# Performance work log

Measured on AMD Instinct MI355X. Metric: run time of the kernel, lower is better.

## Reference

```python
import jax, jax.numpy as jnp
import numpy as np

B, T = 32, 1500
EPROJS, DUNITS = 1024, 1024
AHEADS, DK, DV = 8, 128, 128
SCALING = 1.0 / np.sqrt(DK)


def setup_inputs() -> dict:
    key = jax.random.key(0)
    ks = jax.random.split(key, 8)
    enc_hs_pad = jax.random.normal(ks[0], (B, T, EPROJS), dtype=jnp.float32)
    # lengths in [T//2, T] so every row has at least one valid frame
    enc_hs_len = jax.random.randint(ks[1], (B,), T // 2, T + 1, dtype=jnp.int64)
    dec_z = jax.random.normal(ks[2], (B, DUNITS), dtype=jnp.float32)
    # per-head projection weights (torch.nn.Linear default init scale ~ 1/sqrt(fan_in))
    Wq = jax.random.normal(ks[3], (AHEADS, DUNITS, DK), dtype=jnp.float32) / np.sqrt(DUNITS)
    bq = jax.random.normal(ks[4], (AHEADS, DK), dtype=jnp.float32) / np.sqrt(DUNITS)
    Wk = jax.random.normal(ks[5], (AHEADS, EPROJS, DK), dtype=jnp.float32) / np.sqrt(EPROJS)
    Wv = jax.random.normal(ks[6], (AHEADS, EPROJS, DV), dtype=jnp.float32) / np.sqrt(EPROJS)
    Wo = jax.random.normal(ks[7], (AHEADS * DV, EPROJS), dtype=jnp.float32) / np.sqrt(AHEADS * DV)
    return {"enc_hs_pad": enc_hs_pad, "enc_hs_len": enc_hs_len, "dec_z": dec_z,
            "Wq": Wq, "bq": bq, "Wk": Wk, "Wv": Wv, "Wo": Wo}


def reference(enc_hs_pad, enc_hs_len, dec_z, Wq, bq, Wk, Wv, Wo):
    # pre_compute_k / pre_compute_v, batched over heads
    k = jnp.tanh(jnp.einsum('btd,hdk->bhtk', enc_hs_pad, Wk))   # (B,H,T,DK)
    v = jnp.einsum('btd,hdv->bhtv', enc_hs_pad, Wv)             # (B,H,T,DV)
    q = jnp.tanh(jnp.einsum('bd,hdk->bhk', dec_z, Wq) + bq[None])  # (B,H,DK)
    e = jnp.einsum('bhtk,bhk->bht', k, q)                        # (B,H,T)
    # pad mask: positions >= length are masked with -inf (before scaling, as in source)
    pad = jnp.arange(T)[None, :] >= enc_hs_len[:, None]          # (B,T)
    e = jnp.where(pad[:, None, :], -jnp.inf, e)
    w = jax.nn.softmax(SCALING * e, axis=-1)                     # (B,H,T)
    c = jnp.einsum('bhtv,bht->bhv', v, w)                        # (B,H,DV)
    out = c.reshape(c.shape[0], AHEADS * DV) @ Wo                # (B,EPROJS)
    return out, w
```

## Files before the change

### kernel.cpp

```cpp
#include <hip/hip_runtime.h>
#include <stdint.h>

#define T_SEQ   1500
#define NB      32
#define NH      8
#define SCALING 0.08838834764831845f

typedef __attribute__((ext_vector_type(8))) short short8;
typedef __attribute__((ext_vector_type(16))) float floatx16;

__device__ __forceinline__ uint16_t f2bf(float f) {
    uint32_t u = __float_as_uint(f);
    u += 0x7fffu + ((u >> 16) & 1u);
    return (uint16_t)(u >> 16);
}
__device__ __forceinline__ float fast_tanh(float x) {
    return 1.f - 2.f / (__expf(2.f * x) + 1.f);
}
__device__ __forceinline__ int get_len(const int* L, int b) {
    return (L[1] == 0) ? L[2 * b] : L[b];
}

__global__ __launch_bounds__(256) void k_conv_enc(const float* __restrict__ in,
                                                  uint16_t* __restrict__ out) {
    int i = blockIdx.x * 256 + threadIdx.x;
    const float4* p = (const float4*)in + (size_t)i * 2;
    float4 a = p[0], b = p[1];
    uint4 r;
    r.x = (uint32_t)f2bf(a.x) | ((uint32_t)f2bf(a.y) << 16);
    r.y = (uint32_t)f2bf(a.z) | ((uint32_t)f2bf(a.w) << 16);
    r.z = (uint32_t)f2bf(b.x) | ((uint32_t)f2bf(b.y) << 16);
    r.w = (uint32_t)f2bf(b.z) | ((uint32_t)f2bf(b.w) << 16);
    ((uint4*)out)[i] = r;
}

__global__ __launch_bounds__(128) void k_conv_wkB(const float* __restrict__ Wk,
                                                  uint16_t* __restrict__ Bp) {
    int h = blockIdx.x, g = blockIdx.y;
    int n = threadIdx.x;
    const float* src = Wk + (size_t)h * 131072 + (size_t)g * 8 * 128 + n;
    uint16_t v[8];
#pragma unroll
    for (int e = 0; e < 8; ++e) v[e] = f2bf(src[(size_t)e * 128]);
    uint4 r;
    r.x = (uint32_t)v[0] | ((uint32_t)v[1] << 16);
    r.y = (uint32_t)v[2] | ((uint32_t)v[3] << 16);
    r.z = (uint32_t)v[4] | ((uint32_t)v[5] << 16);
    r.w = (uint32_t)v[6] | ((uint32_t)v[7] << 16);
    *(uint4*)(Bp + (((size_t)h * 128 + g) * 128 + n) * 8) = r;
}

__global__ __launch_bounds__(1024) void k_q(const float* __restrict__ dec_z,
                                            const float* __restrict__ Wq,
                                            const float* __restrict__ bq,
                                            float* __restrict__ q_ws) {
    __shared__ float zs[1024];
    __shared__ float part[8][128];
    int b = blockIdx.x, h = blockIdx.y, tid = threadIdx.x;
    zs[tid] = dec_z[b * 1024 + tid];
    __syncthreads();
    int c = tid & 127, ks = tid >> 7;
    float acc = 0.f;
    const float* wp = Wq + (size_t)h * 131072 + (size_t)ks * 128 * 128 + c;
    const float* zp = zs + ks * 128;
#pragma unroll 16
    for (int d = 0; d < 128; ++d) acc += zp[d] * wp[(size_t)d * 128];
    part[ks][c] = acc;
    __syncthreads();
    if (tid < 128) {
        float a = bq[h * 128 + tid];
#pragma unroll
        for (int k2 = 0; k2 < 8; ++k2) a += part[k2][tid];
        q_ws[(b * 8 + h) * 128 + tid] = fast_tanh(a);
    }
}

__global__ __launch_bounds__(512, 4) void k_gemm_e(const uint16_t* __restrict__ A,
                                                   const uint16_t* __restrict__ Bp,
                                                   const float* __restrict__ q_ws,
                                                   float* __restrict__ e_ws) {
    __shared__ uint16_t As[4][128 * 32];

    const int tid = threadIdx.x;
    const int lane = tid & 63, wv = tid >> 6;
    const int hl = lane >> 5, la = lane & 31;

    const int idx = blockIdx.x;
    const int x = idx & 7;
    const int j = idx >> 3;
    int mt = x * 47 + (j >> 2);
    const int hpair = j & 3;
    if (mt > 374) mt = 374;
    const int m_base = mt * 128;

    const int b0 = m_base / 1500;
    const int b1 = (m_base + 127) / 1500;

    const int wm = wv & 1;
    const int wq = wv >> 1;
    const int h = hpair * 2 + (wq >> 1);
    const int wn = wq & 1;

    const int c0 = wn * 64 + la;
    const float* qp0 = q_ws + (b0 * 8 + h) * 128;
    const float* qp1 = q_ws + (b1 * 8 + h) * 128;
    const float q00 = qp0[c0], q01 = qp0[c0 + 32];
    const float q10 = qp1[c0], q11 = qp1[c0 + 32];

    floatx16 acc[2][2];
#pragma unroll
    for (int i = 0; i < 2; ++i)
#pragma unroll
        for (int jj = 0; jj < 2; ++jj)
#pragma unroll
            for (int r = 0; r < 16; ++r) acc[i][jj][r] = 0.f;

    const char* Ab = (const char*)A;
    char* AsB = (char*)As;
    const short8* Bp8 = (const short8*)Bp + (size_t)h * 16384 + wn * 64 + la;

    short8 br[2][2][2];

    const int dg = lane >> 3;
    const int dj = (lane & 7) ^ dg;
    const int drow = wv * 16 + 2 * dg + (dj >> 2);
    const int du = dj & 3;
    const char* dma_g0 = Ab + (size_t)(m_base + drow) * 2048 + du * 16;

#define DMA_KT(kt)                                                                   \
    {                                                                                \
        const char* ga = dma_g0 + (kt) * 64;                                         \
        char* ldsa = AsB + ((kt) & 3) * 8192 + wv * 1024;                            \
        __builtin_amdgcn_global_load_lds((const __attribute__((address_space(1))) void*)ga, \
                                         (__attribute__((address_space(3))) void*)ldsa, 16, 0, 0); \
    }
#define BLD_KT(kt)                                                                   \
    {                                                                                \
        _Pragma("unroll")                                                            \
        for (int s = 0; s < 2; ++s) {                                                \
            const short8* bg = Bp8 + (size_t)((kt) * 4 + s * 2 + hl) * 128;          \
            br[(kt) & 1][s][0] = bg[0];                                              \
            br[(kt) & 1][s][1] = bg[32];                                             \
        }                                                                            \
    }

    BLD_KT(0);
    DMA_KT(0);
    DMA_KT(1);
    __builtin_amdgcn_s_waitcnt(0x0f71);

#pragma unroll
    for (int kt = 0; kt < 32; ++kt) {
        __builtin_amdgcn_s_barrier();
        if (kt < 31) BLD_KT(kt + 1);
        if (kt < 30) DMA_KT(kt + 2);
#pragma unroll
        for (int s = 0; s < 2; ++s) {
            short8 af[2];
#pragma unroll
            for (int i = 0; i < 2; ++i) {
                int r = wm * 64 + i * 32 + la;
                int p = r >> 1;
                int jsl = (((r & 1) << 2) + s * 2 + hl) ^ (p & 7);
                af[i] = *(const short8*)(AsB + (kt & 3) * 8192 + p * 128 + jsl * 16);
            }
#pragma unroll
            for (int i = 0; i < 2; ++i)
#pragma unroll
                for (int jj = 0; jj < 2; ++jj)
                    acc[i][jj] = __builtin_amdgcn_mfma_f32_32x32x16_bf16(af[i], br[kt & 1][s][jj], acc[i][jj], 0, 0, 0);
        }
        if (kt < 30)
            __builtin_amdgcn_s_waitcnt(0x0f75);
        else if (kt == 30)
            __builtin_amdgcn_s_waitcnt(0x0f74);
    }
#undef DMA_KT
#undef BLD_KT

    __syncthreads();
    float (*ered)[128][2] = (float(*)[128][2])AsB;

    const int lim = (b0 + 1) * 1500 - m_base;
    const int hloc = wq >> 1;
#pragma unroll
    for (int i = 0; i < 2; ++i) {
#pragma unroll
        for (int rg = 0; rg < 16; ++rg) {
            int rowl = wm * 64 + i * 32 + (rg & 3) + 8 * (rg >> 2) + 4 * hl;
            bool second = (rowl >= lim);
            float qa = second ? q10 : q00;
            float qb = second ? q11 : q01;
            float es = fast_tanh(acc[i][0][rg]) * qa + fast_tanh(acc[i][1][rg]) * qb;
            es += __shfl_xor(es, 1);
            es += __shfl_xor(es, 2);
            es += __shfl_xor(es, 4);
            es += __shfl_xor(es, 8);
            es += __shfl_xor(es, 16);
            if (la == 0) ered[hloc][rowl][wn] = es;
        }
    }
    __syncthreads();
    if (tid < 256) {
        int hloc2 = tid >> 7, rowl = tid & 127;
        int rg = m_base + rowl;
        int b = rg / 1500, t = rg - b * 1500;
        e_ws[(b * 8 + hpair * 2 + hloc2) * 1500 + t] = ered[hloc2][rowl][0] + ered[hloc2][rowl][1];
    }
}

__global__ __launch_bounds__(256) void k_softmax(const float* __restrict__ e_ws,
                                                 const int* __restrict__ Lp,
                                                 float* __restrict__ w_out) {
    __shared__ float red[4], red2[4];
    int bh = blockIdx.x, tid = threadIdx.x;
    int len = get_len(Lp, bh >> 3);
    const float* e = e_ws + (size_t)bh * 1500;
    float mx = -1e30f;
    for (int t = tid; t < len; t += 256) mx = fmaxf(mx, e[t]);
#pragma unroll
    for (int o = 1; o < 64; o <<= 1) mx = fmaxf(mx, __shfl_xor(mx, o));
    if ((tid & 63) == 0) red[tid >> 6] = mx;
    __syncthreads();
    mx = fmaxf(fmaxf(red[0], red[1]), fmaxf(red[2], red[3]));
    float s = 0.f;
    for (int t = tid; t < len; t += 256) s += __expf(SCALING * (e[t] - mx));
#pragma unroll
    for (int o = 1; o < 64; o <<= 1) s += __shfl_xor(s, o);
    if ((tid & 63) == 0) red2[tid >> 6] = s;
    __syncthreads();
    float inv = 1.f / (red2[0] + red2[1] + red2[2] + red2[3]);
    for (int t = tid; t < 1500; t += 256) {
        float wv = (t < len) ? __expf(SCALING * (e[t] - mx)) * inv : 0.f;
        w_out[(size_t)bh * 1500 + t] = wv;
    }
}

__global__ __launch_bounds__(256) void k_wsum(const uint16_t* __restrict__ encb,
                                              const float* __restrict__ w,
                                              const int* __restrict__ Lp,
                                              float* __restrict__ s_part) {
    __shared__ float ws_[8][128];
    int dt = blockIdx.x, b = blockIdx.y, p = blockIdx.z;
    int tid = threadIdx.x;
    int len = get_len(Lp, b);
    int t0 = p * 188;
    int t1 = min(min(1500, t0 + 188), len);
    int d0 = (dt * 256 + tid) * 2;
    float a0[8], a1[8];
#pragma unroll
    for (int h = 0; h < 8; ++h) { a0[h] = 0.f; a1[h] = 0.f; }
#define PROCU(u, tl_)                                                        \
    {                                                                        \
        float e0 = __uint_as_float((u) << 16);                               \
        float e1 = __uint_as_float((u) & 0xffff0000u);                       \
        _Pragma("unroll")                                                    \
        for (int hh = 0; hh < 8; ++hh) {                                     \
            float wvv = ws_[hh][tl_];                                        \
            a0[hh] += wvv * e0; a1[hh] += wvv * e1;                          \
        }                                                                    \
    }
    for (int tc = t0; tc < t1; tc += 128) {
        int cl = min(128, t1 - tc);
        __syncthreads();
#pragma unroll
        for (int u = 0; u < 4; ++u) {
            int idx = u * 256 + tid, hh = idx >> 7, tl = idx & 127;
            ws_[hh][tl] = (tl < cl) ? w[(size_t)(b * 8 + hh) * 1500 + tc + tl] : 0.f;
        }
        __syncthreads();
        const uint16_t* ep = encb + ((size_t)b * 1500 + tc) * 1024 + d0;
        int tl = 0;
        for (; tl + 3 < cl; tl += 4) {
            uint32_t u0 = *(const uint32_t*)(ep + (size_t)(tl + 0) * 1024);
            uint32_t u1 = *(const uint32_t*)(ep + (size_t)(tl + 1) * 1024);
            uint32_t u2 = *(const uint32_t*)(ep + (size_t)(tl + 2) * 1024);
            uint32_t u3 = *(const uint32_t*)(ep + (size_t)(tl + 3) * 1024);
            PROCU(u0, tl + 0);
            PROCU(u1, tl + 1);
            PROCU(u2, tl + 2);
            PROCU(u3, tl + 3);
        }
        for (; tl < cl; ++tl) {
            uint32_t u = *(const uint32_t*)(ep + (size_t)tl * 1024);
            PROCU(u, tl);
        }
    }
#undef PROCU
#pragma unroll
    for (int h = 0; h < 8; ++h) {
        float2 v = make_float2(a0[h], a1[h]);
        *(float2*)&s_part[(((size_t)p * 32 + b) * 8 + h) * 1024 + d0] = v;
    }
}

__global__ __launch_bounds__(1024) void k_cv(const float* __restrict__ s_part,
                                             const float* __restrict__ Wv,
                                             float* __restrict__ c_ws) {
    __shared__ float sv[1024];
    __shared__ float part[8][128];
    int b = blockIdx.x, h = blockIdx.y, tid = threadIdx.x;
    {
        float a = 0.f;
#pragma unroll
        for (int p = 0; p < 8; ++p)
            a += s_part[(((size_t)p * 32 + b) * 8 + h) * 1024 + tid];
        sv[tid] = a;
    }
    __syncthreads();
    int c = tid & 127, ks = tid >> 7;
    float acc = 0.f;
    const float* wp = Wv + (size_t)h * 131072 + (size_t)ks * 128 * 128 + c;
    const float* sp = sv + ks * 128;
#pragma unroll 16
    for (int d = 0; d < 128; ++d) acc += sp[d] * wp[(size_t)d * 128];
    part[ks][c] = acc;
    __syncthreads();
    if (tid < 128) {
        float a = 0.f;
#pragma unroll
        for (int k2 = 0; k2 < 8; ++k2) a += part[k2][tid];
        c_ws[(b * 8 + h) * 128 + tid] = a;
    }
}

__global__ __launch_bounds__(1024) void k_out(const float* __restrict__ c_ws,
                                              const float* __restrict__ Wo,
                                              float* __restrict__ outp) {
    __shared__ float cs[1024];
    __shared__ float part[8][128];
    int nt = blockIdx.x, b = blockIdx.y, tid = threadIdx.x;
    cs[tid] = c_ws[b * 1024 + tid];
    __syncthreads();
    int c = tid & 127, ks = tid >> 7;
    float acc = 0.f;
    const float* wp = Wo + (size_t)(ks * 128) * 1024 + nt * 128 + c;
    const float* cp = cs + ks * 128;
#pragma unroll 16
    for (int m = 0; m < 128; ++m) acc += cp[m] * wp[(size_t)m * 1024];
    part[ks][c] = acc;
    __syncthreads();
    if (tid < 128) {
        float a = 0.f;
#pragma unroll
        for (int k2 = 0; k2 < 8; ++k2) a += part[k2][tid];
        outp[(size_t)b * 1024 + nt * 128 + tid] = a;
    }
}

extern "C" void kernel_launch(void* const* d_in, const int* in_sizes, int n_in,
                              void* d_out, int out_size, void* d_ws, size_t ws_size,
                              hipStream_t stream) {
    const float* enc   = (const float*)d_in[0];
    const int*   lens  = (const int*)d_in[1];
    const float* dec_z = (const float*)d_in[2];
    const float* Wq    = (const float*)d_in[3];
    const float* bq    = (const float*)d_in[4];
    const float* Wk    = (const float*)d_in[5];
    const float* Wv    = (const float*)d_in[6];
    const float* Wo    = (const float*)d_in[7];
    float* outp  = (float*)d_out;
    float* w_out = outp + 32768;

    char* ws = (char*)d_ws;
    uint16_t* encb   = (uint16_t*)ws;
    uint16_t* Bp     = (uint16_t*)(ws + 98304000);
    float*    q_ws   = (float*)(ws + 100401152);
    float*    e_ws   = (float*)(ws + 100532224);
    float*    s_part = (float*)(ws + 102068224);
    float*    c_ws   = (float*)(ws + 110456832);
    if (ws_size < 110587904) return;

    k_conv_enc<<<24000, 256, 0, stream>>>(enc, encb);
    k_conv_wkB<<<dim3(8, 128), 128, 0, stream>>>(Wk, Bp);
    k_q<<<dim3(32, 8), 1024, 0, stream>>>(dec_z, Wq, bq, q_ws);
    k_gemm_e<<<1504, 512, 0, stream>>>(encb, Bp, q_ws, e_ws);
    k_softmax<<<256, 256, 0, stream>>>(e_ws, lens, w_out);
    k_wsum<<<dim3(2, 32, 8), 256, 0, stream>>>(encb, w_out, lens, s_part);
    k_cv<<<dim3(32, 8), 1024, 0, stream>>>(s_part, Wv, c_ws);
    k_out<<<dim3(8, 32), 1024, 0, stream>>>(c_ws, Wo, outp);
}
```

Measured before the change: 475.7 us.

## Drop bf16 pre-conversion of encoder; convert fp32 tiles in-register inside GEMM

Removes the separate kernel that converted the fp32 encoder states to bf16 and instead streams the fp32 encoder straight into LDS in the e-GEMM, converting to bf16 with packed cvt instructions just before the MFMA. The weighted-sum kernel also reads the fp32 encoder directly. This avoids one full read of the encoder plus a write and re-read of its bf16 copy, but the GEMM and wsum kernels now move twice the bytes per tile and use double the LDS, and the GEMM inner loop gains extra conversion ALU work.

Measured after the change: 476.8 us. Within noise of the previous version (+0.2%).

```diff
diff --git a/kernel.cpp b/kernel.cpp
--- a/kernel.cpp
+++ b/kernel.cpp
@@ -9,29 +9,16 @@
 typedef __attribute__((ext_vector_type(8))) short short8;
 typedef __attribute__((ext_vector_type(16))) float floatx16;
 
-__device__ __forceinline__ uint16_t f2bf(float f) {
-    uint32_t u = __float_as_uint(f);
-    u += 0x7fffu + ((u >> 16) & 1u);
-    return (uint16_t)(u >> 16);
-}
 __device__ __forceinline__ float fast_tanh(float x) {
     return 1.f - 2.f / (__expf(2.f * x) + 1.f);
 }
 __device__ __forceinline__ int get_len(const int* L, int b) {
     return (L[1] == 0) ? L[2 * b] : L[b];
 }
-
-__global__ __launch_bounds__(256) void k_conv_enc(const float* __restrict__ in,
-                                                  uint16_t* __restrict__ out) {
-    int i = blockIdx.x * 256 + threadIdx.x;
-    const float4* p = (const float4*)in + (size_t)i * 2;
-    float4 a = p[0], b = p[1];
-    uint4 r;
-    r.x = (uint32_t)f2bf(a.x) | ((uint32_t)f2bf(a.y) << 16);
-    r.y = (uint32_t)f2bf(a.z) | ((uint32_t)f2bf(a.w) << 16);
-    r.z = (uint32_t)f2bf(b.x) | ((uint32_t)f2bf(b.y) << 16);
-    r.w = (uint32_t)f2bf(b.z) | ((uint32_t)f2bf(b.w) << 16);
-    ((uint4*)out)[i] = r;
+__device__ __forceinline__ uint32_t cvtpk(float lo, float hi) {
+    uint32_t r;
+    asm("v_cvt_pk_bf16_f32 %0, %1, %2" : "=v"(r) : "v"(lo), "v"(hi));
+    return r;
 }
 
 __global__ __launch_bounds__(128) void k_conv_wkB(const float* __restrict__ Wk,
@@ -39,14 +26,14 @@
     int h = blockIdx.x, g = blockIdx.y;
     int n = threadIdx.x;
     const float* src = Wk + (size_t)h * 131072 + (size_t)g * 8 * 128 + n;
-    uint16_t v[8];
-#pragma unroll
-    for (int e = 0; e < 8; ++e) v[e] = f2bf(src[(size_t)e * 128]);
+    float f[8];
+#pragma unroll
+    for (int e = 0; e < 8; ++e) f[e] = src[(size_t)e * 128];
     uint4 r;
-    r.x = (uint32_t)v[0] | ((uint32_t)v[1] << 16);
-    r.y = (uint32_t)v[2] | ((uint32_t)v[3] << 16);
-    r.z = (uint32_t)v[4] | ((uint32_t)v[5] << 16);
-    r.w = (uint32_t)v[6] | ((uint32_t)v[7] << 16);
+    r.x = cvtpk(f[0], f[1]);
+    r.y = cvtpk(f[2], f[3]);
+    r.z = cvtpk(f[4], f[5]);
+    r.w = cvtpk(f[6], f[7]);
     *(uint4*)(Bp + (((size_t)h * 128 + g) * 128 + n) * 8) = r;
 }
 
@@ -75,11 +62,11 @@
     }
 }
 
-__global__ __launch_bounds__(512, 4) void k_gemm_e(const uint16_t* __restrict__ A,
+__global__ __launch_bounds__(512, 4) void k_gemm_e(const float* __restrict__ A,
                                                    const uint16_t* __restrict__ Bp,
                                                    const float* __restrict__ q_ws,
                                                    float* __restrict__ e_ws) {
-    __shared__ uint16_t As[4][128 * 32];
+    __shared__ float4 As4[4 * 1024];
 
     const int tid = threadIdx.x;
     const int lane = tid & 63, wv = tid >> 6;
@@ -116,23 +103,24 @@
             for (int r = 0; r < 16; ++r) acc[i][jj][r] = 0.f;
 
     const char* Ab = (const char*)A;
-    char* AsB = (char*)As;
+    char* AsB = (char*)As4;
     const short8* Bp8 = (const short8*)Bp + (size_t)h * 16384 + wn * 64 + la;
 
     short8 br[2][2][2];
 
     const int dg = lane >> 3;
     const int dj = (lane & 7) ^ dg;
-    const int drow = wv * 16 + 2 * dg + (dj >> 2);
-    const int du = dj & 3;
-    const char* dma_g0 = Ab + (size_t)(m_base + drow) * 2048 + du * 16;
+    const char* dma_g0 = Ab + (size_t)(m_base + wv * 16 + dg) * 4096 + dj * 16;
 
 #define DMA_KT(kt)                                                                   \
     {                                                                                \
-        const char* ga = dma_g0 + (kt) * 64;                                         \
-        char* ldsa = AsB + ((kt) & 3) * 8192 + wv * 1024;                            \
-        __builtin_amdgcn_global_load_lds((const __attribute__((address_space(1))) void*)ga, \
-                                         (__attribute__((address_space(3))) void*)ldsa, 16, 0, 0); \
+        _Pragma("unroll")                                                            \
+        for (int it = 0; it < 2; ++it) {                                             \
+            const char* ga = dma_g0 + (size_t)it * 8 * 4096 + (kt) * 128;            \
+            char* ldsa = AsB + ((kt) & 3) * 16384 + wv * 2048 + it * 1024;           \
+            __builtin_amdgcn_global_load_lds((const __attribute__((address_space(1))) void*)ga, \
+                                             (__attribute__((address_space(3))) void*)ldsa, 16, 0, 0); \
+        }                                                                            \
     }
 #define BLD_KT(kt)                                                                   \
     {                                                                                \
@@ -147,7 +135,7 @@
     BLD_KT(0);
     DMA_KT(0);
     DMA_KT(1);
-    __builtin_amdgcn_s_waitcnt(0x0f71);
+    __builtin_amdgcn_s_waitcnt(0x0f72);
 
 #pragma unroll
     for (int kt = 0; kt < 32; ++kt) {
@@ -156,22 +144,26 @@
         if (kt < 30) DMA_KT(kt + 2);
 #pragma unroll
         for (int s = 0; s < 2; ++s) {
-            short8 af[2];
 #pragma unroll
             for (int i = 0; i < 2; ++i) {
                 int r = wm * 64 + i * 32 + la;
-                int p = r >> 1;
-                int jsl = (((r & 1) << 2) + s * 2 + hl) ^ (p & 7);
-                af[i] = *(const short8*)(AsB + (kt & 3) * 8192 + p * 128 + jsl * 16);
+                const char* rowp = AsB + (kt & 3) * 16384 + r * 128;
+                int sl0 = (s * 4 + hl * 2) ^ (r & 7);
+                float4 fA = *(const float4*)(rowp + sl0 * 16);
+                float4 fB = *(const float4*)(rowp + (sl0 ^ 1) * 16);
+                uint4 uu;
+                uu.x = cvtpk(fA.x, fA.y);
+                uu.y = cvtpk(fA.z, fA.w);
+                uu.z = cvtpk(fB.x, fB.y);
+                uu.w = cvtpk(fB.z, fB.w);
+                short8 af = *reinterpret_cast<short8*>(&uu);
+#pragma unroll
+                for (int jj = 0; jj < 2; ++jj)
+                    acc[i][jj] = __builtin_amdgcn_mfma_f32_32x32x16_bf16(af, br[kt & 1][s][jj], acc[i][jj], 0, 0, 0);
             }
-#pragma unroll
-            for (int i = 0; i < 2; ++i)
-#pragma unroll
-                for (int jj = 0; jj < 2; ++jj)
-                    acc[i][jj] = __builtin_amdgcn_mfma_f32_32x32x16_bf16(af[i], br[kt & 1][s][jj], acc[i][jj], 0, 0, 0);
         }
         if (kt < 30)
-            __builtin_amdgcn_s_waitcnt(0x0f75);
+            __builtin_amdgcn_s_waitcnt(0x0f76);
         else if (kt == 30)
             __builtin_amdgcn_s_waitcnt(0x0f74);
     }
@@ -236,7 +228,7 @@
     }
 }
 
-__global__ __launch_bounds__(256) void k_wsum(const uint16_t* __restrict__ encb,
+__global__ __launch_bounds__(256) void k_wsum(const float* __restrict__ enc,
                                               const float* __restrict__ w,
                                               const int* __restrict__ Lp,
                                               float* __restrict__ s_part) {
@@ -252,8 +244,8 @@
     for (int h = 0; h < 8; ++h) { a0[h] = 0.f; a1[h] = 0.f; }
 #define PROCU(u, tl_)                                                        \
     {                                                                        \
-        float e0 = __uint_as_float((u) << 16);                               \
-        float e1 = __uint_as_float((u) & 0xffff0000u);                       \
+        float e0 = (u).x;                                                    \
+        float e1 = (u).y;                                                    \
         _Pragma("unroll")                                                    \
         for (int hh = 0; hh < 8; ++hh) {                                     \
             float wvv = ws_[hh][tl_];                                        \
@@ -269,20 +261,20 @@
             ws_[hh][tl] = (tl < cl) ? w[(size_t)(b * 8 + hh) * 1500 + tc + tl] : 0.f;
         }
         __syncthreads();
-        const uint16_t* ep = encb + ((size_t)b * 1500 + tc) * 1024 + d0;
+        const float* ep = enc + ((size_t)b * 1500 + tc) * 1024 + d0;
         int tl = 0;
         for (; tl + 3 < cl; tl += 4) {
-            uint32_t u0 = *(const uint32_t*)(ep + (size_t)(tl + 0) * 1024);
-            uint32_t u1 = *(const uint32_t*)(ep + (size_t)(tl + 1) * 1024);
-            uint32_t u2 = *(const uint32_t*)(ep + (size_t)(tl + 2) * 1024);
-            uint32_t u3 = *(const uint32_t*)(ep + (size_t)(tl + 3) * 1024);
+            float2 u0 = *(const float2*)(ep + (size_t)(tl + 0) * 1024);
+            float2 u1 = *(const float2*)(ep + (size_t)(tl + 1) * 1024);
+            float2 u2 = *(const float2*)(ep + (size_t)(tl + 2) * 1024);
+            float2 u3 = *(const float2*)(ep + (size_t)(tl + 3) * 1024);
             PROCU(u0, tl + 0);
             PROCU(u1, tl + 1);
             PROCU(u2, tl + 2);
             PROCU(u3, tl + 3);
         }
         for (; tl < cl; ++tl) {
-            uint32_t u = *(const uint32_t*)(ep + (size_t)tl * 1024);
+            float2 u = *(const float2*)(ep + (size_t)tl * 1024);
             PROCU(u, tl);
         }
     }
@@ -363,20 +355,18 @@
     float* w_out = outp + 32768;
 
     char* ws = (char*)d_ws;
-    uint16_t* encb   = (uint16_t*)ws;
-    uint16_t* Bp     = (uint16_t*)(ws + 98304000);
-    float*    q_ws   = (float*)(ws + 100401152);
-    float*    e_ws   = (float*)(ws + 100532224);
-    float*    s_part = (float*)(ws + 102068224);
-    float*    c_ws   = (float*)(ws + 110456832);
-    if (ws_size < 110587904) return;
-
-    k_conv_enc<<<24000, 256, 0, stream>>>(enc, encb);
+    uint16_t* Bp     = (uint16_t*)ws;
+    float*    q_ws   = (float*)(ws + 2097152);
+    float*    e_ws   = (float*)(ws + 2228224);
+    float*    s_part = (float*)(ws + 3764224);
+    float*    c_ws   = (float*)(ws + 12152832);
+    if (ws_size < 12283904) return;
+
     k_conv_wkB<<<dim3(8, 128), 128, 0, stream>>>(Wk, Bp);
     k_q<<<dim3(32, 8), 1024, 0, stream>>>(dec_z, Wq, bq, q_ws);
-    k_gemm_e<<<1504, 512, 0, stream>>>(encb, Bp, q_ws, e_ws);
+    k_gemm_e<<<1504, 512, 0, stream>>>(enc, Bp, q_ws, e_ws);
     k_softmax<<<256, 256, 0, stream>>>(e_ws, lens, w_out);
-    k_wsum<<<dim3(2, 32, 8), 256, 0, stream>>>(encb, w_out, lens, s_part);
+    k_wsum<<<dim3(2, 32, 8), 256, 0, stream>>>(enc, w_out, lens, s_part);
     k_cv<<<dim3(32, 8), 1024, 0, stream>>>(s_part, Wv, c_ws);
     k_out<<<dim3(8, 32), 1024, 0, stream>>>(c_ws, Wo, outp);
 }
```
